# Kernel tuning notes

Measured on AMD Instinct MI355X. Metric: run time of the kernel, lower is better.

## Reference

```python
import jax, jax.numpy as jnp
import numpy as np

NUM_CLASSES = 80
THR_CONF = 0.02
THR_NMS = 0.5
IMG_SIZE = 416.0


def setup_inputs() -> dict:
    key = jax.random.key(0)
    pyolos = jax.random.normal(key, (4, 1 + NUM_CLASSES + 4, 26, 26), dtype=jnp.float32)
    return {"pyolos": pyolos}


def _decode(pyolos):
    # pyolos: [B, C, H, W] -> [B, HW, C] (matches view+permute in torch)
    B, C, H, W = pyolos.shape
    p = pyolos.reshape(B, C, H * W).transpose(0, 2, 1)
    pconf = jax.nn.sigmoid(p[:, :, 0])                      # [B, HW]
    cls = jax.nn.softmax(p[:, :, 1:1 + NUM_CLASSES], -1)
    cls_conf = cls.max(-1)
    plabels = jnp.argmax(cls, -1)
    pscores = cls_conf * pconf                              # [B, HW]
    t = p[:, :, 1 + NUM_CLASSES:]                           # [B, HW, 4]
    # f_mershgrid(h, w, is_rowcol=False): flat (x=col, y=row) order
    ys, xs = jnp.meshgrid(jnp.arange(H), jnp.arange(W), indexing='ij')
    grid = jnp.stack([xs.reshape(-1), ys.reshape(-1)], -1).astype(pyolos.dtype)  # [HW, 2]
    hw = jnp.array([H, W], dtype=pyolos.dtype)
    xy = (jax.nn.sigmoid(t[:, :, :2]) + grid) / hw          # true_divide by (h, w)
    wh = jnp.exp(t[:, :, 2:4]) / IMG_SIZE
    ltrb = jnp.concatenate([xy - wh * 0.5, xy + wh * 0.5], -1)
    ltrb = jnp.clip(ltrb, 0.0, 1.0)
    return pscores, plabels + 1, ltrb


def _pairwise_iou(b):
    # b: [N, 4] ltrb
    area = (b[:, 2] - b[:, 0]) * (b[:, 3] - b[:, 1])        # [N]
    lt = jnp.maximum(b[:, None, :2], b[None, :, :2])        # [N, N, 2]
    rb = jnp.minimum(b[:, None, 2:], b[None, :, 2:])
    wh = jnp.clip(rb - lt, 0.0)
    inter = wh[..., 0] * wh[..., 1]
    return inter / (area[:, None] + area[None, :] - inter + 1e-9)


def _nms_keep(boxes_off, scores_masked, mask):
    # Greedy class/batch-aware NMS via offset boxes; fixed-shape keep mask.
    N = boxes_off.shape[0]
    order = jnp.argsort(-scores_masked)
    b_s = boxes_off[order]
    keep0 = mask[order]
    iou = _pairwise_iou(b_s)                                # [N, N]
    idx = jnp.arange(N)

    def step(keep, i):
        sup = keep[i] & (iou[i] > THR_NMS) & (idx > i)
        return keep & ~sup, None

    keep_s, _ = jax.lax.scan(step, keep0, idx)
    return jnp.zeros(N, dtype=bool).at[order].set(keep_s)


def reference(pyolos):
    B, C, H, W = pyolos.shape
    pscores, plabels, ltrb = _decode(pyolos)
    N = B * H * W
    scores = pscores.reshape(N)
    labels = plabels.reshape(N)
    boxes = ltrb.reshape(N, 4)
    ids_batch = jnp.repeat(jnp.arange(B), H * W)
    mask = scores > THR_CONF
    # label_nms: NMS only within same (batch, label) -> offset coordinates
    off = (ids_batch * (NUM_CLASSES + 2) + labels).astype(boxes.dtype) * 2.0
    boxes_off = boxes + off[:, None]
    scores_masked = jnp.where(mask, scores, 0.0)
    keep = _nms_keep(boxes_off, scores_masked, mask)
    # Fixed-shape analogue of (ids_batch2, boxes2, labels2, scores2): keep mask selects
    return ids_batch, boxes, labels, scores, keep
```

## Files before the change

kernel.cpp:

```cpp
#include <hip/hip_runtime.h>


#define BATCH 4
#define HW 676
#define GW 26
#define NC 80
#define NTOT 2704

__device__ __forceinline__ float fast_exp(float x) { return __expf(x); }

__device__ __forceinline__ float fast_sigmoid(float x) {
    return 1.0f / (1.0f + __expf(-x));
}

__device__ __forceinline__ float opaque(float x) {
    asm volatile("" : "+v"(x));
    return x;
}

__global__ void yolo_decode_kernel(const float* __restrict__ in,
                                   float* __restrict__ out) {
    int idx = blockIdx.x * blockDim.x + threadIdx.x;
    if (idx >= NTOT) return;
    int b = idx / HW;
    int n = idx - b * HW;
    const float* p = in + (size_t)b * 85 * HW + n;

    float pconf = fast_sigmoid(p[0]);

    float m = p[1 * HW];
    int arg = 0;
    for (int c = 1; c < NC; ++c) {
        float v = p[(1 + c) * HW];
        if (v > m) { m = v; arg = c; }
    }
    float s = 0.0f;
    for (int c = 0; c < NC; ++c) {
        s += fast_exp(p[(1 + c) * HW] - m);
    }
    float cls_conf = 1.0f / s;
    float score = cls_conf * pconf;

    float tx = p[81 * HW], ty = p[82 * HW], tw = p[83 * HW], th = p[84 * HW];
    float gx = (float)(n % GW);
    float gy = (float)(n / GW);
    float cx = (fast_sigmoid(tx) + gx) * (1.0f / 26.0f);
    float cy = (fast_sigmoid(ty) + gy) * (1.0f / 26.0f);
    float w = fast_exp(tw) * (1.0f / 416.0f);
    float h = fast_exp(th) * (1.0f / 416.0f);
    float l = fminf(fmaxf(cx - w * 0.5f, 0.0f), 1.0f);
    float t = fminf(fmaxf(cy - h * 0.5f, 0.0f), 1.0f);
    float r = fminf(fmaxf(cx + w * 0.5f, 0.0f), 1.0f);
    float bt = fminf(fmaxf(cy + h * 0.5f, 0.0f), 1.0f);

    out[idx] = (float)b;
    float* ob = out + NTOT + (size_t)idx * 4;
    ob[0] = l; ob[1] = t; ob[2] = r; ob[3] = bt;
    out[(size_t)NTOT * 5 + idx] = (float)(arg + 1);
    out[(size_t)NTOT * 6 + idx] = score;
    out[(size_t)NTOT * 7 + idx] = 0.0f;
}

__global__ void __launch_bounds__(256) yolo_nms_wave_kernel(float* __restrict__ out) {
    const int lane = threadIdx.x & 63;
    const int wid = threadIdx.x >> 6;
    const int g = blockIdx.x * 4 + wid;
    const int b = g / NC;
    const int cls = (g % NC) + 1;

    const float* boxes = out + NTOT;
    const float* labels = out + (size_t)NTOT * 5;
    const float* scores = out + (size_t)NTOT * 6;
    float* keep = out + (size_t)NTOT * 7;

    __shared__ int sIdx[4][64];
    __shared__ float sSc[4][64];

    const float fcls = (float)cls;
    const int base = b * HW;

    int k = 0;
    const unsigned long long below = (lane == 0) ? 0ull : (~0ull >> (64 - lane));
    for (int it = 0; it < 11; ++it) {
        int cell = it * 64 + lane;
        bool pred = false;
        float scv = 0.0f;
        int gi = base + cell;
        if (cell < HW) {
            scv = scores[gi];
            pred = (labels[gi] == fcls) && (scv > 0.02f);
        }
        unsigned long long mask = __ballot(pred);
        if (pred) {
            int pos = k + __popcll(mask & below);
            if (pos < 64) { sIdx[wid][pos] = gi; sSc[wid][pos] = scv; }
        }
        k += __popcll(mask);
    }
    if (k > 64) k = 64;

    if (k == 0) return;

    const bool valid = lane < k;
    int my_idx = valid ? sIdx[wid][lane] : 0;
    float my_sc = valid ? sSc[wid][lane] : 0.0f;

    int rank = 0;
    for (int mm = 0; mm < k; ++mm) {
        float om = __shfl(my_sc, mm);
        if (valid && ((om > my_sc) || (om == my_sc && mm < lane))) ++rank;
    }
    if (!valid) rank = 127;

    float off = (float)((b * (NC + 2) + cls) * 2);
    float x1 = 0, y1 = 0, x2 = 0, y2 = 0, area = 0;
    if (valid) {
        const float* bp = boxes + (size_t)my_idx * 4;
        x1 = bp[0] + off; y1 = bp[1] + off;
        x2 = bp[2] + off; y2 = bp[3] + off;
        area = opaque((x2 - x1) * (y2 - y1));
    }

    bool alive = valid;
    for (int r = 0; r < k; ++r) {
        unsigned long long rm = __ballot(rank == r);
        int src = (int)(__ffsll((long long)rm) - 1);
        bool src_alive = ((__ballot(alive) >> src) & 1ull) != 0ull;
        float bx1 = __shfl(x1, src), by1 = __shfl(y1, src);
        float bx2 = __shfl(x2, src), by2 = __shfl(y2, src);
        float bar = __shfl(area, src);
        if (src_alive && alive && rank > r) {
            float ltx = fmaxf(bx1, x1), lty = fmaxf(by1, y1);
            float rbx = fminf(bx2, x2), rby = fminf(by2, y2);
            float wx = fmaxf(rbx - ltx, 0.0f);
            float wy = fmaxf(rby - lty, 0.0f);
            float inter = opaque(wx * wy);
            float iou = inter / (bar + area - inter + 1e-9f);
            if (iou > 0.5f) alive = false;
        }
    }
    if (valid && alive) keep[my_idx] = 1.0f;
}

extern "C" void kernel_launch(void* const* d_in, const int* in_sizes, int n_in,
                              void* d_out, int out_size, void* d_ws, size_t ws_size,
                              hipStream_t stream) {
    const float* in = (const float*)d_in[0];
    float* out = (float*)d_out;
    (void)in_sizes; (void)n_in; (void)out_size; (void)d_ws; (void)ws_size;

    hipLaunchKernelGGL(yolo_decode_kernel, dim3((NTOT + 255) / 256), dim3(256),
                       0, stream, in, out);
    hipLaunchKernelGGL(yolo_nms_wave_kernel, dim3(80), dim3(256), 0, stream, out);
}
```

Measured before the change: 70.93 us.

## Fuse decode and per-class NMS into one kernel per batch image

Replaces the separate decode and NMS kernels with a single kernel that launches one 1024-thread block per batch image. Decoded scores, labels and boxes stay in shared memory, and 16 waves each run NMS for 5 classes. This removes a kernel launch and the global-memory round trip between the two stages. In exchange only 4 blocks run, so parallelism drops sharply, and each wave now does its 5 classes one after another.

```diff
diff --git a/kernel.cpp b/kernel.cpp
--- a/kernel.cpp
+++ b/kernel.cpp
@@ -6,6 +6,7 @@
 #define GW 26
 #define NC 80
 #define NTOT 2704
+#define NWAVE 16
 
 __device__ __forceinline__ float fast_exp(float x) { return __expf(x); }
 
@@ -18,128 +19,128 @@
     return x;
 }
 
-__global__ void yolo_decode_kernel(const float* __restrict__ in,
-                                   float* __restrict__ out) {
-    int idx = blockIdx.x * blockDim.x + threadIdx.x;
-    if (idx >= NTOT) return;
-    int b = idx / HW;
-    int n = idx - b * HW;
-    const float* p = in + (size_t)b * 85 * HW + n;
+__global__ void __launch_bounds__(1024) yolo_fused_kernel(
+        const float* __restrict__ in, float* __restrict__ out) {
+    __shared__ float sSc[HW];
+    __shared__ int sLab[HW];
+    __shared__ float sBox[HW][4];
+    __shared__ int cIdx[NWAVE][64];
+    __shared__ float cSc[NWAVE][64];
 
-    float pconf = fast_sigmoid(p[0]);
+    const int b = blockIdx.x;
+    const int t = threadIdx.x;
 
-    float m = p[1 * HW];
-    int arg = 0;
-    for (int c = 1; c < NC; ++c) {
-        float v = p[(1 + c) * HW];
-        if (v > m) { m = v; arg = c; }
+    if (t < HW) {
+        const float* p = in + (size_t)b * 85 * HW + t;
+
+        float pconf = fast_sigmoid(p[0]);
+
+        float m = p[1 * HW];
+        int arg = 0;
+        for (int c = 1; c < NC; ++c) {
+            float v = p[(1 + c) * HW];
+            if (v > m) { m = v; arg = c; }
+        }
+        float s = 0.0f;
+        for (int c = 0; c < NC; ++c) {
+            s += fast_exp(p[(1 + c) * HW] - m);
+        }
+        float score = (1.0f / s) * pconf;
+
+        float tx = p[81 * HW], ty = p[82 * HW], tw = p[83 * HW], th = p[84 * HW];
+        float gx = (float)(t % GW);
+        float gy = (float)(t / GW);
+        float cx = (fast_sigmoid(tx) + gx) * (1.0f / 26.0f);
+        float cy = (fast_sigmoid(ty) + gy) * (1.0f / 26.0f);
+        float w = fast_exp(tw) * (1.0f / 416.0f);
+        float h = fast_exp(th) * (1.0f / 416.0f);
+        float l = fminf(fmaxf(cx - w * 0.5f, 0.0f), 1.0f);
+        float tt = fminf(fmaxf(cy - h * 0.5f, 0.0f), 1.0f);
+        float r = fminf(fmaxf(cx + w * 0.5f, 0.0f), 1.0f);
+        float bt = fminf(fmaxf(cy + h * 0.5f, 0.0f), 1.0f);
+
+        int gi = b * HW + t;
+        out[gi] = (float)b;
+        float* ob = out + NTOT + (size_t)gi * 4;
+        ob[0] = l; ob[1] = tt; ob[2] = r; ob[3] = bt;
+        out[(size_t)NTOT * 5 + gi] = (float)(arg + 1);
+        out[(size_t)NTOT * 6 + gi] = score;
+        out[(size_t)NTOT * 7 + gi] = 0.0f;
+
+        sSc[t] = score;
+        sLab[t] = arg + 1;
+        sBox[t][0] = l; sBox[t][1] = tt; sBox[t][2] = r; sBox[t][3] = bt;
     }
-    float s = 0.0f;
-    for (int c = 0; c < NC; ++c) {
-        s += fast_exp(p[(1 + c) * HW] - m);
+    __syncthreads();
+
+    const int lane = t & 63;
+    const int wid = t >> 6;
+    float* keep = out + (size_t)NTOT * 7;
+    const unsigned long long below =
+        (lane == 0) ? 0ull : (~0ull >> (64 - lane));
+
+    for (int q = 0; q < 5; ++q) {
+        const int g = wid * 5 + q;
+        const int cls = g + 1;
+
+        int k = 0;
+        for (int it = 0; it < 11; ++it) {
+            int cell = it * 64 + lane;
+            bool pred = false;
+            float scv = 0.0f;
+            if (cell < HW) {
+                scv = sSc[cell];
+                pred = (sLab[cell] == cls) && (scv > 0.02f);
+            }
+            unsigned long long mask = __ballot(pred);
+            if (pred) {
+                int pos = k + __popcll(mask & below);
+                if (pos < 64) { cIdx[wid][pos] = cell; cSc[wid][pos] = scv; }
+            }
+            k += __popcll(mask);
+        }
+        if (k > 64) k = 64;
+        if (k == 0) continue;
+
+        const bool valid = lane < k;
+        int my_cell = valid ? cIdx[wid][lane] : 0;
+        float my_sc = valid ? cSc[wid][lane] : 0.0f;
+
+        int rank = 0;
+        for (int mm = 0; mm < k; ++mm) {
+            float om = __shfl(my_sc, mm);
+            if (valid && ((om > my_sc) || (om == my_sc && mm < lane))) ++rank;
+        }
+        if (!valid) rank = 127;
+
+        float off = (float)((b * (NC + 2) + cls) * 2);
+        float x1 = 0, y1 = 0, x2 = 0, y2 = 0, area = 0;
+        if (valid) {
+            x1 = sBox[my_cell][0] + off; y1 = sBox[my_cell][1] + off;
+            x2 = sBox[my_cell][2] + off; y2 = sBox[my_cell][3] + off;
+            area = opaque((x2 - x1) * (y2 - y1));
+        }
+
+        bool alive = valid;
+        for (int r = 0; r < k; ++r) {
+            unsigned long long rm = __ballot(rank == r);
+            int src = (int)(__ffsll((long long)rm) - 1);
+            bool src_alive = ((__ballot(alive) >> src) & 1ull) != 0ull;
+            float bx1 = __shfl(x1, src), by1 = __shfl(y1, src);
+            float bx2 = __shfl(x2, src), by2 = __shfl(y2, src);
+            float bar = __shfl(area, src);
+            if (src_alive && alive && rank > r) {
+                float ltx = fmaxf(bx1, x1), lty = fmaxf(by1, y1);
+                float rbx = fminf(bx2, x2), rby = fminf(by2, y2);
+                float wx = fmaxf(rbx - ltx, 0.0f);
+                float wy = fmaxf(rby - lty, 0.0f);
+                float inter = opaque(wx * wy);
+                float iou = inter / (bar + area - inter + 1e-9f);
+                if (iou > 0.5f) alive = false;
+            }
+        }
+        if (valid && alive) keep[b * HW + my_cell] = 1.0f;
     }
-    float cls_conf = 1.0f / s;
-    float score = cls_conf * pconf;
-
-    float tx = p[81 * HW], ty = p[82 * HW], tw = p[83 * HW], th = p[84 * HW];
-    float gx = (float)(n % GW);
-    float gy = (float)(n / GW);
-    float cx = (fast_sigmoid(tx) + gx) * (1.0f / 26.0f);
-    float cy = (fast_sigmoid(ty) + gy) * (1.0f / 26.0f);
-    float w = fast_exp(tw) * (1.0f / 416.0f);
-    float h = fast_exp(th) * (1.0f / 416.0f);
-    float l = fminf(fmaxf(cx - w * 0.5f, 0.0f), 1.0f);
-    float t = fminf(fmaxf(cy - h * 0.5f, 0.0f), 1.0f);
-    float r = fminf(fmaxf(cx + w * 0.5f, 0.0f), 1.0f);
-    float bt = fminf(fmaxf(cy + h * 0.5f, 0.0f), 1.0f);
-
-    out[idx] = (float)b;
-    float* ob = out + NTOT + (size_t)idx * 4;
-    ob[0] = l; ob[1] = t; ob[2] = r; ob[3] = bt;
-    out[(size_t)NTOT * 5 + idx] = (float)(arg + 1);
-    out[(size_t)NTOT * 6 + idx] = score;
-    out[(size_t)NTOT * 7 + idx] = 0.0f;
-}
-
-__global__ void __launch_bounds__(256) yolo_nms_wave_kernel(float* __restrict__ out) {
-    const int lane = threadIdx.x & 63;
-    const int wid = threadIdx.x >> 6;
-    const int g = blockIdx.x * 4 + wid;
-    const int b = g / NC;
-    const int cls = (g % NC) + 1;
-
-    const float* boxes = out + NTOT;
-    const float* labels = out + (size_t)NTOT * 5;
-    const float* scores = out + (size_t)NTOT * 6;
-    float* keep = out + (size_t)NTOT * 7;
-
-    __shared__ int sIdx[4][64];
-    __shared__ float sSc[4][64];
-
-    const float fcls = (float)cls;
-    const int base = b * HW;
-
-    int k = 0;
-    const unsigned long long below = (lane == 0) ? 0ull : (~0ull >> (64 - lane));
-    for (int it = 0; it < 11; ++it) {
-        int cell = it * 64 + lane;
-        bool pred = false;
-        float scv = 0.0f;
-        int gi = base + cell;
-        if (cell < HW) {
-            scv = scores[gi];
-            pred = (labels[gi] == fcls) && (scv > 0.02f);
-        }
-        unsigned long long mask = __ballot(pred);
-        if (pred) {
-            int pos = k + __popcll(mask & below);
-            if (pos < 64) { sIdx[wid][pos] = gi; sSc[wid][pos] = scv; }
-        }
-        k += __popcll(mask);
-    }
-    if (k > 64) k = 64;
-
-    if (k == 0) return;
-
-    const bool valid = lane < k;
-    int my_idx = valid ? sIdx[wid][lane] : 0;
-    float my_sc = valid ? sSc[wid][lane] : 0.0f;
-
-    int rank = 0;
-    for (int mm = 0; mm < k; ++mm) {
-        float om = __shfl(my_sc, mm);
-        if (valid && ((om > my_sc) || (om == my_sc && mm < lane))) ++rank;
-    }
-    if (!valid) rank = 127;
-
-    float off = (float)((b * (NC + 2) + cls) * 2);
-    float x1 = 0, y1 = 0, x2 = 0, y2 = 0, area = 0;
-    if (valid) {
-        const float* bp = boxes + (size_t)my_idx * 4;
-        x1 = bp[0] + off; y1 = bp[1] + off;
-        x2 = bp[2] + off; y2 = bp[3] + off;
-        area = opaque((x2 - x1) * (y2 - y1));
-    }
-
-    bool alive = valid;
-    for (int r = 0; r < k; ++r) {
-        unsigned long long rm = __ballot(rank == r);
-        int src = (int)(__ffsll((long long)rm) - 1);
-        bool src_alive = ((__ballot(alive) >> src) & 1ull) != 0ull;
-        float bx1 = __shfl(x1, src), by1 = __shfl(y1, src);
-        float bx2 = __shfl(x2, src), by2 = __shfl(y2, src);
-        float bar = __shfl(area, src);
-        if (src_alive && alive && rank > r) {
-            float ltx = fmaxf(bx1, x1), lty = fmaxf(by1, y1);
-            float rbx = fminf(bx2, x2), rby = fminf(by2, y2);
-            float wx = fmaxf(rbx - ltx, 0.0f);
-            float wy = fmaxf(rby - lty, 0.0f);
-            float inter = opaque(wx * wy);
-            float iou = inter / (bar + area - inter + 1e-9f);
-            if (iou > 0.5f) alive = false;
-        }
-    }
-    if (valid && alive) keep[my_idx] = 1.0f;
 }
 
 extern "C" void kernel_launch(void* const* d_in, const int* in_sizes, int n_in,
@@ -149,7 +150,6 @@
     float* out = (float*)d_out;
     (void)in_sizes; (void)n_in; (void)out_size; (void)d_ws; (void)ws_size;
 
-    hipLaunchKernelGGL(yolo_decode_kernel, dim3((NTOT + 255) / 256), dim3(256),
-                       0, stream, in, out);
-    hipLaunchKernelGGL(yolo_nms_wave_kernel, dim3(80), dim3(256), 0, stream, out);
+    hipLaunchKernelGGL(yolo_fused_kernel, dim3(BATCH), dim3(1024), 0, stream,
+                       in, out);
 }
```

Result: slower. 87.39 us (+23.2%).

## Split decode class softmax across four waves per cell with shared-memory reduction

Applied to the files above, without the earlier changes.

The decode kernel now gives each group of 64 cells four waves, each handling 20 of the 80 class logits. Partial max/argmax and partial exp-sums are combined through shared memory, and the first wave writes the outputs. This spreads the long serial 80-class loop over more threads and blocks (43 instead of 11), so more loads are in flight. The cost is two block barriers and some shared-memory traffic.

```diff
diff --git a/kernel.cpp b/kernel.cpp
--- a/kernel.cpp
+++ b/kernel.cpp
@@ -6,8 +6,7 @@
 #define GW 26
 #define NC 80
 #define NTOT 2704
-
-__device__ __forceinline__ float fast_exp(float x) { return __expf(x); }
+#define CPB 64
 
 __device__ __forceinline__ float fast_sigmoid(float x) {
     return 1.0f / (1.0f + __expf(-x));
@@ -18,47 +17,84 @@
     return x;
 }
 
-__global__ void yolo_decode_kernel(const float* __restrict__ in,
-                                   float* __restrict__ out) {
-    int idx = blockIdx.x * blockDim.x + threadIdx.x;
-    if (idx >= NTOT) return;
-    int b = idx / HW;
-    int n = idx - b * HW;
+__global__ void __launch_bounds__(256) yolo_decode_kernel(
+        const float* __restrict__ in, float* __restrict__ out) {
+    __shared__ float pMax[4][CPB];
+    __shared__ int pArg[4][CPB];
+    __shared__ float pSum[4][CPB];
+
+    const int lane = threadIdx.x & 63;
+    const int q = threadIdx.x >> 6;
+    const int idx = blockIdx.x * CPB + lane;
+    const bool valid = idx < NTOT;
+
+    int b = 0, n = 0;
+    if (valid) { b = idx / HW; n = idx - b * HW; }
     const float* p = in + (size_t)b * 85 * HW + n;
 
-    float pconf = fast_sigmoid(p[0]);
+    float v[20];
+    if (valid) {
+#pragma unroll
+        for (int j = 0; j < 20; ++j) v[j] = p[(1 + 20 * q + j) * HW];
+    } else {
+#pragma unroll
+        for (int j = 0; j < 20; ++j) v[j] = 0.0f;
+    }
+    float c0 = 0, tx = 0, ty = 0, tw = 0, th = 0;
+    if (q == 0 && valid) {
+        c0 = p[0];
+        tx = p[81 * HW]; ty = p[82 * HW];
+        tw = p[83 * HW]; th = p[84 * HW];
+    }
 
-    float m = p[1 * HW];
+    float m = v[0];
     int arg = 0;
-    for (int c = 1; c < NC; ++c) {
-        float v = p[(1 + c) * HW];
-        if (v > m) { m = v; arg = c; }
+#pragma unroll
+    for (int j = 1; j < 20; ++j)
+        if (v[j] > m) { m = v[j]; arg = j; }
+    pMax[q][lane] = m;
+    pArg[q][lane] = 20 * q + arg;
+    __syncthreads();
+
+    const float m0 = pMax[0][lane], m1 = pMax[1][lane];
+    const float m2 = pMax[2][lane], m3 = pMax[3][lane];
+    const float gm = fmaxf(fmaxf(m0, m1), fmaxf(m2, m3));
+
+    float s = 0.0f;
+#pragma unroll
+    for (int j = 0; j < 20; ++j) s += __expf(v[j] - gm);
+    pSum[q][lane] = s;
+    __syncthreads();
+
+    if (q == 0 && valid) {
+        int argf = pArg[0][lane];
+        float bb = m0;
+        if (m1 > bb) { bb = m1; argf = pArg[1][lane]; }
+        if (m2 > bb) { bb = m2; argf = pArg[2][lane]; }
+        if (m3 > bb) { bb = m3; argf = pArg[3][lane]; }
+
+        float stot = pSum[0][lane] + pSum[1][lane] + pSum[2][lane] +
+                     pSum[3][lane];
+        float score = (1.0f / stot) * fast_sigmoid(c0);
+
+        float gx = (float)(n % GW);
+        float gy = (float)(n / GW);
+        float cx = (fast_sigmoid(tx) + gx) * (1.0f / 26.0f);
+        float cy = (fast_sigmoid(ty) + gy) * (1.0f / 26.0f);
+        float w = __expf(tw) * (1.0f / 416.0f);
+        float h = __expf(th) * (1.0f / 416.0f);
+        float l = fminf(fmaxf(cx - w * 0.5f, 0.0f), 1.0f);
+        float t = fminf(fmaxf(cy - h * 0.5f, 0.0f), 1.0f);
+        float r = fminf(fmaxf(cx + w * 0.5f, 0.0f), 1.0f);
+        float bt = fminf(fmaxf(cy + h * 0.5f, 0.0f), 1.0f);
+
+        out[idx] = (float)b;
+        float* ob = out + NTOT + (size_t)idx * 4;
+        ob[0] = l; ob[1] = t; ob[2] = r; ob[3] = bt;
+        out[(size_t)NTOT * 5 + idx] = (float)(argf + 1);
+        out[(size_t)NTOT * 6 + idx] = score;
+        out[(size_t)NTOT * 7 + idx] = 0.0f;
     }
-    float s = 0.0f;
-    for (int c = 0; c < NC; ++c) {
-        s += fast_exp(p[(1 + c) * HW] - m);
-    }
-    float cls_conf = 1.0f / s;
-    float score = cls_conf * pconf;
-
-    float tx = p[81 * HW], ty = p[82 * HW], tw = p[83 * HW], th = p[84 * HW];
-    float gx = (float)(n % GW);
-    float gy = (float)(n / GW);
-    float cx = (fast_sigmoid(tx) + gx) * (1.0f / 26.0f);
-    float cy = (fast_sigmoid(ty) + gy) * (1.0f / 26.0f);
-    float w = fast_exp(tw) * (1.0f / 416.0f);
-    float h = fast_exp(th) * (1.0f / 416.0f);
-    float l = fminf(fmaxf(cx - w * 0.5f, 0.0f), 1.0f);
-    float t = fminf(fmaxf(cy - h * 0.5f, 0.0f), 1.0f);
-    float r = fminf(fmaxf(cx + w * 0.5f, 0.0f), 1.0f);
-    float bt = fminf(fmaxf(cy + h * 0.5f, 0.0f), 1.0f);
-
-    out[idx] = (float)b;
-    float* ob = out + NTOT + (size_t)idx * 4;
-    ob[0] = l; ob[1] = t; ob[2] = r; ob[3] = bt;
-    out[(size_t)NTOT * 5 + idx] = (float)(arg + 1);
-    out[(size_t)NTOT * 6 + idx] = score;
-    out[(size_t)NTOT * 7 + idx] = 0.0f;
 }
 
 __global__ void __launch_bounds__(256) yolo_nms_wave_kernel(float* __restrict__ out) {
@@ -98,7 +134,6 @@
         k += __popcll(mask);
     }
     if (k > 64) k = 64;
-
     if (k == 0) return;
 
     const bool valid = lane < k;
@@ -149,7 +184,7 @@
     float* out = (float*)d_out;
     (void)in_sizes; (void)n_in; (void)out_size; (void)d_ws; (void)ws_size;
 
-    hipLaunchKernelGGL(yolo_decode_kernel, dim3((NTOT + 255) / 256), dim3(256),
-                       0, stream, in, out);
+    hipLaunchKernelGGL(yolo_decode_kernel, dim3((NTOT + CPB - 1) / CPB),
+                       dim3(256), 0, stream, in, out);
     hipLaunchKernelGGL(yolo_nms_wave_kernel, dim3(80), dim3(256), 0, stream, out);
 }
```

After: 62.95 us. -11.3%, faster.
